# Optimization experiments

Measured on AMD Instinct MI355X. Metric: run time of the kernel, lower is better.

The kernel has to match this reference:

```python
import jax, jax.numpy as jnp
import numpy as np

B, T_MEM, T_TGT = 32, 256, 128
E = H = 512          # embed_size == hidden_size == memory feature dim (required by module math)
V = 10000            # vocab size


def setup_inputs() -> dict:
    key = jax.random.key(0)
    ks = jax.random.split(key, 10)
    s = 0.05
    return {
        "memory": jax.random.normal(ks[0], (B, T_MEM, E), dtype=jnp.float32),
        "tgt": jax.random.randint(ks[1], (B, T_TGT), 0, V),
        "emb_in": jax.random.normal(ks[2], (V, E), dtype=jnp.float32) * s,
        "W_ih": jax.random.normal(ks[3], (4 * H, E + H), dtype=jnp.float32) * s,
        "W_hh": jax.random.normal(ks[4], (4 * H, H), dtype=jnp.float32) * s,
        "b_ih": jax.random.normal(ks[5], (4 * H,), dtype=jnp.float32) * s,
        "b_hh": jax.random.normal(ks[6], (4 * H,), dtype=jnp.float32) * s,
        "W_out": jax.random.normal(ks[7], (V, H), dtype=jnp.float32) * s,
        "b_out": jax.random.normal(ks[8], (V,), dtype=jnp.float32) * s,
    }


def reference(memory, tgt, emb_in, W_ih, W_hh, b_ih, b_hh, W_out, b_out):
    # memory: (B, T_mem, E); tgt: (B, T_tgt) int
    Bq, Tm, Ed = memory.shape
    Hd = W_hh.shape[1]
    scale = 1.0 / jnp.sqrt(jnp.asarray(Ed, dtype=memory.dtype))

    x_emb = emb_in[tgt]                       # (B, T_tgt, E) teacher-forced inputs
    x_seq = jnp.swapaxes(x_emb, 0, 1)         # (T_tgt, B, E) for scan

    def step(carry, x_t):
        h, c = carry                          # (B, H), (B, H)
        # scaled dot-product attention: query=h, keys=values=memory
        scores = jnp.einsum('be,bte->bt', h, memory) * scale
        attn = jax.nn.softmax(scores, axis=-1)
        context = jnp.einsum('bt,bte->be', attn, memory)   # (B, E)
        inp = jnp.concatenate([context, x_t], axis=-1)     # (B, E + E_embed)
        gates = inp @ W_ih.T + b_ih + h @ W_hh.T + b_hh    # (B, 4H)
        i, f, g, o = jnp.split(gates, 4, axis=-1)          # torch LSTMCell gate order
        c_new = jax.nn.sigmoid(f) * c + jax.nn.sigmoid(i) * jnp.tanh(g)
        h_new = jax.nn.sigmoid(o) * jnp.tanh(c_new)
        logits = h_new @ W_out.T + b_out                   # (B, V)
        return (h_new, c_new), logits

    h0 = jnp.zeros((Bq, Hd), dtype=memory.dtype)
    c0 = jnp.zeros((Bq, Hd), dtype=memory.dtype)
    _, logits_seq = jax.lax.scan(step, (h0, c0), x_seq)    # (T_tgt, B, V)
    return jnp.swapaxes(logits_seq, 0, 1)                  # (B, T_tgt, V)
```

## Files before the change

### kernel.cpp

```cpp
#include <hip/hip_runtime.h>
#include <stdint.h>

#define TT 128

typedef __attribute__((ext_vector_type(8))) short short8;
typedef __attribute__((ext_vector_type(4))) float f32x4;
typedef __attribute__((ext_vector_type(4))) uint32_t u32x4;

__device__ __forceinline__ float blo(uint32_t u){ union{uint32_t i; float f;} v; v.i = u << 16; return v.f; }
__device__ __forceinline__ float bhi(uint32_t u){ union{uint32_t i; float f;} v; v.i = u & 0xffff0000u; return v.f; }
__device__ __forceinline__ float bf2f(uint16_t u){ union{uint32_t i; float f;} v; v.i = ((uint32_t)u) << 16; return v.f; }
__device__ __forceinline__ uint16_t f2bf(float f){
  union{float f; uint32_t i;} v; v.f = f;
  uint32_t r = v.i + 0x7fffu + ((v.i >> 16) & 1u);
  return (uint16_t)(r >> 16);
}
__device__ __forceinline__ uint32_t bfpack(float a, float b) {
  return (uint32_t)f2bf(a) | ((uint32_t)f2bf(b) << 16);
}
__device__ __forceinline__ void xstore(uint32_t* p, uint32_t v) {
  __hip_atomic_store(p, v, __ATOMIC_RELAXED, __HIP_MEMORY_SCOPE_AGENT);
}
__device__ __forceinline__ uint32_t xload(const uint32_t* p) {
  return __hip_atomic_load(p, __ATOMIC_RELAXED, __HIP_MEMORY_SCOPE_AGENT);
}
__device__ __forceinline__ void xstore64(unsigned long long* p, unsigned long long v) {
  __hip_atomic_store(p, v, __ATOMIC_RELAXED, __HIP_MEMORY_SCOPE_AGENT);
}
__device__ __forceinline__ unsigned long long xload64(const unsigned long long* p) {
  return __hip_atomic_load(p, __ATOMIC_RELAXED, __HIP_MEMORY_SCOPE_AGENT);
}
__device__ __forceinline__ void xstoref(float* p, float v) {
  __hip_atomic_store(p, v, __ATOMIC_RELAXED, __HIP_MEMORY_SCOPE_AGENT);
}
__device__ __forceinline__ float xloadf(const float* p) {
  return __hip_atomic_load(p, __ATOMIC_RELAXED, __HIP_MEMORY_SCOPE_AGENT);
}

__global__ __launch_bounds__(256) void k_prep_mem(const float* __restrict__ mem,
                                                  uint32_t* __restrict__ memK,
                                                  uint32_t* __restrict__ memT) {
  int idx = blockIdx.x * 256 + threadIdx.x;
  if (idx < 2097152) {
    int e2 = idx & 255, k = (idx >> 8) & 255, b = idx >> 16;
    const float* p = mem + ((size_t)(b * 256 + k)) * 512 + e2 * 2;
    memK[idx] = bfpack(p[0], p[1]);
  } else {
    int j = idx - 2097152;
    int k = j & 255, e2 = (j >> 8) & 255, b = j >> 16;
    const float* p = mem + ((size_t)(b * 256 + k)) * 512 + e2 * 2;
    memT[j] = bfpack(p[0], p[1]);
  }
}

__global__ __launch_bounds__(256) void k_prep_wsl(const float* __restrict__ W_ih, const float* __restrict__ W_hh,
                                                  uint32_t* __restrict__ Wsl) {
  int idx = blockIdx.x * 256 + threadIdx.x;
  int kk = idx & 3, t = (idx >> 2) & 255, kc = (idx >> 10) & 127, s = idx >> 17;
  int j = (t & 3) * 512 + s * 64 + (t >> 2);
  int k0 = kc * 8 + kk * 2;
  float w0 = (k0 < 512) ? W_ih[(size_t)j * 1024 + k0] : W_hh[(size_t)j * 512 + (k0 - 512)];
  float w1 = (k0 + 1 < 512) ? W_ih[(size_t)j * 1024 + k0 + 1] : W_hh[(size_t)j * 512 + (k0 + 1 - 512)];
  Wsl[idx] = bfpack(w0, w1);
}

__global__ __launch_bounds__(256) void k_prep_wx(const float* __restrict__ W_ih,
                                                 const float* __restrict__ b_ih, const float* __restrict__ b_hh,
                                                 uint16_t* __restrict__ Wxp, float* __restrict__ biasp) {
  int idx = blockIdx.x * 256 + threadIdx.x;
  int k = idx & 511, j = idx >> 9;
  Wxp[idx] = f2bf(W_ih[(size_t)j * 1024 + 512 + k]);
  if (k == 0) biasp[j] = b_ih[j] + b_hh[j];
}

__global__ __launch_bounds__(256) void k_prep_wo(const float* __restrict__ W_out, uint16_t* __restrict__ WoP) {
  int idx = blockIdx.x * 256 + threadIdx.x;
  if (idx < 5120000) WoP[idx] = f2bf(W_out[idx]);
  else WoP[idx] = 0;
}

__global__ __launch_bounds__(256) void k_gather_x(const float* __restrict__ emb, const int* __restrict__ tgt,
                                                  uint16_t* __restrict__ Axg) {
  int idx = blockIdx.x * 256 + threadIdx.x;
  int k = idx & 511, m = idx >> 9;
  Axg[idx] = f2bf(emb[(size_t)tgt[m] * 512 + k]);
}

template<int MODE>
__global__ __launch_bounds__(256) void gemm_bt(const uint16_t* __restrict__ A, const uint16_t* __restrict__ B,
                                               const float* __restrict__ bias, void* __restrict__ Cout,
                                               int K, int Nreal, int ldc, int tilesN) {
  __shared__ __align__(16) uint16_t As[128 * 32];
  __shared__ __align__(16) uint16_t Bs[128 * 32];
  const int tid = threadIdx.x;
  const int wv = tid >> 6, lane = tid & 63;
  const int tm = blockIdx.x / tilesN, tn = blockIdx.x % tilesN;
  const int wr = wv >> 1, wc = wv & 1;

  f32x4 acc[4][4];
#pragma unroll
  for (int m = 0; m < 4; ++m)
#pragma unroll
    for (int n = 0; n < 4; ++n) acc[m][n] = (f32x4){0.f, 0.f, 0.f, 0.f};

  const int frow = lane & 15;
  const int fk = (lane >> 4) << 3;
  const int srow = lane >> 2;
  const int skof = (lane & 3) << 3;

  const uint16_t* Abase = A + (size_t)tm * 128 * K;
  const uint16_t* Bbase = B + (size_t)tn * 128 * K;

  for (int k0 = 0; k0 < K; k0 += 32) {
    __syncthreads();
#pragma unroll
    for (int i = 0; i < 2; ++i) {
      const int chunk = wv * 2 + i;
      const int row = chunk * 16 + srow;
      const uint16_t* ga = Abase + (size_t)row * K + k0 + skof;
      const uint16_t* gb = Bbase + (size_t)row * K + k0 + skof;
      __builtin_amdgcn_global_load_lds((const __attribute__((address_space(1))) uint32_t*)(const void*)ga,
                                       (__attribute__((address_space(3))) uint32_t*)(void*)(As + chunk * 512),
                                       16, 0, 0);
      __builtin_amdgcn_global_load_lds((const __attribute__((address_space(1))) uint32_t*)(const void*)gb,
                                       (__attribute__((address_space(3))) uint32_t*)(void*)(Bs + chunk * 512),
                                       16, 0, 0);
    }
    __syncthreads();
    short8 af[4], bfr[4];
#pragma unroll
    for (int m = 0; m < 4; ++m) af[m] = *(const short8*)(As + (wr * 64 + m * 16 + frow) * 32 + fk);
#pragma unroll
    for (int n = 0; n < 4; ++n) bfr[n] = *(const short8*)(Bs + (wc * 64 + n * 16 + frow) * 32 + fk);
#pragma unroll
    for (int m = 0; m < 4; ++m)
#pragma unroll
      for (int n = 0; n < 4; ++n)
        acc[m][n] = __builtin_amdgcn_mfma_f32_16x16x32_bf16(af[m], bfr[n], acc[m][n], 0, 0, 0);
  }

  const int crow = (lane >> 4) << 2;
  const int ccol = lane & 15;
#pragma unroll
  for (int n = 0; n < 4; ++n) {
    const int gcol = tn * 128 + wc * 64 + n * 16 + ccol;
    if (gcol < Nreal) {
      const float bv = bias[gcol];
#pragma unroll
      for (int m = 0; m < 4; ++m) {
#pragma unroll
        for (int j = 0; j < 4; ++j) {
          const int grow = tm * 128 + wr * 64 + m * 16 + crow + j;
          const float v = acc[m][n][j] + bv;
          if (MODE == 0) ((float*)Cout)[(size_t)grow * ldc + gcol] = v;
          else {
            int q = gcol >> 9, r = gcol & 511;
            int pos = ((r >> 6) << 8) + ((r & 63) << 2) + q;
            ((uint16_t*)Cout)[(size_t)grow * ldc + pos] = f2bf(v);
          }
        }
      }
    }
  }
}

__global__ __launch_bounds__(512, 1) void recur_kernel(
    const uint32_t* __restrict__ memK, const uint32_t* __restrict__ memT,
    const uint32_t* __restrict__ Wsl, const uint16_t* __restrict__ Xgp,
    unsigned long long* __restrict__ ugl, float* __restrict__ zgl,
    uint32_t* __restrict__ hgl, uint16_t* __restrict__ hA, uint32_t* __restrict__ flags) {
  __shared__ __align__(16) uint32_t mTl[2][8192];
  __shared__ __align__(16) uint32_t mKl[2][8192];
  __shared__ __align__(16) uint32_t hx[2][256];
  __shared__ __align__(16) float xf[2][1024];
  __shared__ float red[256];
  __shared__ float rux[512], ruy[512];
  __shared__ float accs[512];
  __shared__ float el[32];

  const int g = blockIdx.x;
  const int s = g & 7, pp = g >> 3;
  const int tid = threadIdx.x;
  const int lane = tid & 63;
  const int wv = tid >> 6;
  const int sub = tid & 31, p = tid >> 5;
  const int row = tid & 255, half = tid >> 8;

  const uint32_t* wrow = Wsl + ((size_t)s << 17) + row * 4;

#pragma unroll
  for (int bi = 0; bi < 2; ++bi) {
    const int b = pp + bi * 16;
    const uint32_t* mTb = memT + ((size_t)b << 16);
    const uint32_t* mKb = memK + ((size_t)b << 16) + ((size_t)(32 * s) << 8);
    for (int j = tid; j < 8192; j += 512) {
      mKl[bi][j] = mKb[j];
      int e2 = j >> 5, kk = j & 31;
      mTl[bi][j] = mTb[e2 * 256 + 32 * s + kk];
    }
  }
  float c[2] = {0.f, 0.f};
  if (tid < 256) { hx[0][tid] = 0u; hx[1][tid] = 0u; }
  xf[0][tid] = 0.f; xf[0][512 + tid] = 0.f;
  xf[1][tid] = 0.f; xf[1][512 + tid] = 0.f;
  __syncthreads();

  for (int t = 0; t < TT; ++t) {
#pragma unroll
    for (int bi = 0; bi < 2; ++bi) {
      const int b = pp + bi * 16;
      {
        float sc = 0.f;
#pragma unroll
        for (int i = 0; i < 16; ++i) {
          uint32_t mw = mTl[bi][(p + (i << 4)) * 32 + sub];
          uint32_t hw = hx[bi][p + (i << 4)];
          sc = fmaf(blo(mw), blo(hw), sc);
          sc = fmaf(bhi(mw), bhi(hw), sc);
        }
        sc += __shfl_xor(sc, 32);
        if (lane < 32) red[wv * 32 + lane] = sc;
      }
      __syncthreads();
      if (tid < 32) {
        float sf = red[tid] + red[32 + tid] + red[64 + tid] + red[96 + tid]
                 + red[128 + tid] + red[160 + tid] + red[192 + tid] + red[224 + tid];
        float e = __expf(sf * 0.044194173824159216f);
        el[tid] = e;
        float z = e;
        z += __shfl_xor(z, 16); z += __shfl_xor(z, 8);
        z += __shfl_xor(z, 4);  z += __shfl_xor(z, 2); z += __shfl_xor(z, 1);
        if (tid == 0) xstoref(&zgl[(b << 3) + s], z);
      }
      __syncthreads();
      {
        float ux = 0.f, uy = 0.f;
        const int k0 = half * 16;
#pragma unroll
        for (int kk = 0; kk < 16; ++kk) {
          uint32_t mw = mKl[bi][(k0 + kk) * 256 + row];
          float e = el[k0 + kk];
          ux = fmaf(blo(mw), e, ux);
          uy = fmaf(bhi(mw), e, uy);
        }
        rux[tid] = ux; ruy[tid] = uy;
      }
      __syncthreads();
      if (tid < 256) {
        union { float f[2]; unsigned long long u; } pk;
        pk.f[0] = rux[tid] + rux[tid + 256];
        pk.f[1] = ruy[tid] + ruy[tid + 256];
        xstore64(&ugl[(((size_t)b << 3) + s << 8) + tid], pk.u);
      }
      __syncthreads();
      if (tid == 0) xstore(&flags[b * 32 + s], (uint32_t)(2 * t + 1));
    }
#pragma unroll
    for (int bi = 0; bi < 2; ++bi) {
      const int b = pp + bi * 16;
      if (tid < 64) {
        int v;
        do {
          __builtin_amdgcn_s_sleep(2);
          v = (tid < 8) ? (int)xload(&flags[b * 32 + tid]) : (2 * t + 1);
        } while (__any(v < 2 * t + 1));
      }
      __syncthreads();
      {
        float zsum = 0.f;
        if (tid < 256) {
#pragma unroll
          for (int q = 0; q < 8; ++q) zsum += xloadf(&zgl[(b << 3) + q]);
        }
        float ux = 0.f, uy = 0.f;
        const int q0 = half * 4;
#pragma unroll
        for (int q = 0; q < 4; ++q) {
          union { float f[2]; unsigned long long u; } pk;
          pk.u = xload64(&ugl[(((size_t)b << 3) + (q0 + q) << 8) + row]);
          ux += pk.f[0]; uy += pk.f[1];
        }
        rux[tid] = ux; ruy[tid] = uy;
        __syncthreads();
        if (tid < 256) {
          float rz = 1.f / zsum;
          xf[bi][2 * tid]     = (rux[tid] + rux[tid + 256]) * rz;
          xf[bi][2 * tid + 1] = (ruy[tid] + ruy[tid + 256]) * rz;
        }
      }
      __syncthreads();
      {
        float acc = (half == 0) ? bf2f(Xgp[((size_t)b * TT + t) * 2048 + (s << 8) + row]) : 0.f;
        const int kcb = half * 64;
#pragma unroll 8
        for (int j = 0; j < 64; ++j) {
          const int kc = kcb + j;
          u32x4 w4 = *(const u32x4*)(wrow + kc * 1024);
          f32x4 xa = *(const f32x4*)(xf[bi] + kc * 8);
          f32x4 xb = *(const f32x4*)(xf[bi] + kc * 8 + 4);
          acc = fmaf(blo(w4.x), xa.x, acc); acc = fmaf(bhi(w4.x), xa.y, acc);
          acc = fmaf(blo(w4.y), xa.z, acc); acc = fmaf(bhi(w4.y), xa.w, acc);
          acc = fmaf(blo(w4.z), xb.x, acc); acc = fmaf(bhi(w4.z), xb.y, acc);
          acc = fmaf(blo(w4.w), xb.z, acc); acc = fmaf(bhi(w4.w), xb.w, acc);
        }
        accs[tid] = acc;
      }
      __syncthreads();
      if (tid < 256) {
        float tot = accs[tid] + accs[tid + 256];
        int lbase = lane & ~3;
        float gi = __shfl(tot, lbase, 64);
        float gf = __shfl(tot, lbase + 1, 64);
        float gg = __shfl(tot, lbase + 2, 64);
        float go = __shfl(tot, lbase + 3, 64);
        c[bi] = (1.f / (1.f + __expf(-gf))) * c[bi] + (1.f / (1.f + __expf(-gi))) * tanhf(gg);
        float hn = (1.f / (1.f + __expf(-go))) * tanhf(c[bi]);
        float hn4 = __shfl(hn, (lane & ~7) + 4, 64);
        if ((tid & 7) == 0) {
          uint32_t hp = bfpack(hn, hn4);
          int r2 = (s << 5) + (tid >> 3);
          xstore(&hgl[(b << 8) + r2], hp);
          ((uint32_t*)hA)[((size_t)b * TT + t) * 256 + r2] = hp;
        }
      }
      __syncthreads();
      if (tid == 0) xstore(&flags[b * 32 + s], (uint32_t)(2 * t + 2));
    }
#pragma unroll
    for (int bi = 0; bi < 2; ++bi) {
      const int b = pp + bi * 16;
      if (tid < 64) {
        int v;
        do {
          __builtin_amdgcn_s_sleep(2);
          v = (tid < 8) ? (int)xload(&flags[b * 32 + tid]) : (2 * t + 2);
        } while (__any(v < 2 * t + 2));
      }
      __syncthreads();
      if (tid < 256) {
        uint32_t hp = xload(&hgl[(b << 8) + tid]);
        hx[bi][tid] = hp;
        xf[bi][512 + 2 * tid] = blo(hp);
        xf[bi][513 + 2 * tid] = bhi(hp);
      }
    }
    __syncthreads();
  }
}

extern "C" void kernel_launch(void* const* d_in, const int* in_sizes, int n_in,
                              void* d_out, int out_size, void* d_ws, size_t ws_size,
                              hipStream_t stream) {
  const float* memory = (const float*)d_in[0];
  const int*   tgt    = (const int*)d_in[1];
  const float* emb_in = (const float*)d_in[2];
  const float* W_ih   = (const float*)d_in[3];
  const float* W_hh   = (const float*)d_in[4];
  const float* b_ih   = (const float*)d_in[5];
  const float* b_hh   = (const float*)d_in[6];
  const float* W_out  = (const float*)d_in[7];
  const float* b_out  = (const float*)d_in[8];
  float* out = (float*)d_out;
  char* ws = (char*)d_ws;

  uint32_t* memK  = (uint32_t*)(ws);
  uint32_t* memT  = (uint32_t*)(ws + 8388608);
  uint32_t* Wsl   = (uint32_t*)(ws + 16777216);
  uint16_t* Wxp   = (uint16_t*)(ws + 20971520);
  float*    biasp = (float*)(ws + 23068672);
  uint16_t* WoP   = (uint16_t*)(ws + 23076864);
  uint16_t* Axg   = (uint16_t*)(ws + 33431552);
  uint16_t* Xgp   = (uint16_t*)(ws + 37625856);
  uint16_t* hA    = (uint16_t*)(ws + 54403072);
  uint32_t* hgl   = (uint32_t*)(ws + 58597376);
  float*    zgl   = (float*)(ws + 58630144);
  uint32_t* flags = (uint32_t*)(ws + 58662912);
  unsigned long long* ugl = (unsigned long long*)Axg;

  hipMemsetAsync(flags, 0, 4096, stream);

  k_prep_mem<<<16384, 256, 0, stream>>>(memory, memK, memT);
  k_prep_wsl<<<4096, 256, 0, stream>>>(W_ih, W_hh, Wsl);
  k_prep_wx<<<4096, 256, 0, stream>>>(W_ih, b_ih, b_hh, Wxp, biasp);
  k_prep_wo<<<20224, 256, 0, stream>>>(W_out, WoP);
  k_gather_x<<<8192, 256, 0, stream>>>(emb_in, tgt, Axg);

  gemm_bt<1><<<32 * 16, 256, 0, stream>>>(Axg, Wxp, biasp, Xgp, 512, 2048, 2048, 16);

  recur_kernel<<<128, 512, 0, stream>>>(memK, memT, Wsl, Xgp, ugl, zgl, hgl, hA, flags);

  gemm_bt<0><<<32 * 79, 256, 0, stream>>>(hA, WoP, b_out, out, 512, 10000, 10000, 79);
}
```

Measured before the change: 2.127 ms.

## Split recurrence across 256 blocks with shared LSTM weight pass for two batches

The persistent recurrence kernel now runs on 256 blocks instead of 128, each owning 16 memory rows and 32 hidden units for two batch rows. Memory is read straight from global/L2 rather than staged in LDS. The gate matvec is fused so each weight load serves both batch rows, halving weight traffic per block. The cost is twice as many blocks taking part in the cross-block flag synchronisation each step, plus uncached memory reads.

```diff
diff --git a/kernel.cpp b/kernel.cpp
--- a/kernel.cpp
+++ b/kernel.cpp
@@ -53,15 +53,15 @@
   }
 }
 
-__global__ __launch_bounds__(256) void k_prep_wsl(const float* __restrict__ W_ih, const float* __restrict__ W_hh,
-                                                  uint32_t* __restrict__ Wsl) {
+__global__ __launch_bounds__(256) void k_prep_wsl2(const float* __restrict__ W_ih, const float* __restrict__ W_hh,
+                                                   uint32_t* __restrict__ Wsl2) {
   int idx = blockIdx.x * 256 + threadIdx.x;
-  int kk = idx & 3, t = (idx >> 2) & 255, kc = (idx >> 10) & 127, s = idx >> 17;
-  int j = (t & 3) * 512 + s * 64 + (t >> 2);
+  int kk = idx & 3, t2 = (idx >> 2) & 127, kc = (idx >> 9) & 127, sg = idx >> 16;
+  int j = (t2 & 3) * 512 + sg * 32 + (t2 >> 2);
   int k0 = kc * 8 + kk * 2;
   float w0 = (k0 < 512) ? W_ih[(size_t)j * 1024 + k0] : W_hh[(size_t)j * 512 + (k0 - 512)];
   float w1 = (k0 + 1 < 512) ? W_ih[(size_t)j * 1024 + k0 + 1] : W_hh[(size_t)j * 512 + (k0 + 1 - 512)];
-  Wsl[idx] = bfpack(w0, w1);
+  Wsl2[idx] = bfpack(w0, w1);
 }
 
 __global__ __launch_bounds__(256) void k_prep_wx(const float* __restrict__ W_ih,
@@ -166,79 +166,75 @@
 
 __global__ __launch_bounds__(512, 1) void recur_kernel(
     const uint32_t* __restrict__ memK, const uint32_t* __restrict__ memT,
-    const uint32_t* __restrict__ Wsl, const uint16_t* __restrict__ Xgp,
+    const uint32_t* __restrict__ Wsl2, const uint16_t* __restrict__ Xgp,
     unsigned long long* __restrict__ ugl, float* __restrict__ zgl,
     uint32_t* __restrict__ hgl, uint16_t* __restrict__ hA, uint32_t* __restrict__ flags) {
-  __shared__ __align__(16) uint32_t mTl[2][8192];
-  __shared__ __align__(16) uint32_t mKl[2][8192];
   __shared__ __align__(16) uint32_t hx[2][256];
   __shared__ __align__(16) float xf[2][1024];
-  __shared__ float red[256];
+  __shared__ float red[128];
   __shared__ float rux[512], ruy[512];
-  __shared__ float accs[512];
-  __shared__ float el[32];
+  __shared__ float accsA[512], accsB[512];
+  __shared__ float el[16];
 
   const int g = blockIdx.x;
-  const int s = g & 7, pp = g >> 3;
+  const int sg = g & 15, pp = g >> 4;
+  const int b0 = pp, b1 = pp + 16;
   const int tid = threadIdx.x;
   const int lane = tid & 63;
   const int wv = tid >> 6;
-  const int sub = tid & 31, p = tid >> 5;
+  const int kl = tid & 15, eg = tid >> 4;
   const int row = tid & 255, half = tid >> 8;
-
-  const uint32_t* wrow = Wsl + ((size_t)s << 17) + row * 4;
-
-#pragma unroll
-  for (int bi = 0; bi < 2; ++bi) {
-    const int b = pp + bi * 16;
-    const uint32_t* mTb = memT + ((size_t)b << 16);
-    const uint32_t* mKb = memK + ((size_t)b << 16) + ((size_t)(32 * s) << 8);
-    for (int j = tid; j < 8192; j += 512) {
-      mKl[bi][j] = mKb[j];
-      int e2 = j >> 5, kk = j & 31;
-      mTl[bi][j] = mTb[e2 * 256 + 32 * s + kk];
-    }
-  }
-  float c[2] = {0.f, 0.f};
+  const int t2 = tid & 127, h4 = tid >> 7;
+
+  const uint32_t* wr2 = Wsl2 + ((size_t)sg << 16) + t2 * 4;
+  const int rD = 32 * sg + (t2 >> 2), qD = t2 & 3;
+  const int posD = ((rD >> 6) << 8) + ((rD & 63) << 2) + qD;
+
+  float cS = 0.f;
   if (tid < 256) { hx[0][tid] = 0u; hx[1][tid] = 0u; }
   xf[0][tid] = 0.f; xf[0][512 + tid] = 0.f;
   xf[1][tid] = 0.f; xf[1][512 + tid] = 0.f;
   __syncthreads();
 
   for (int t = 0; t < TT; ++t) {
+    const int T1 = 2 * t + 1, T2 = 2 * t + 2;
 #pragma unroll
     for (int bi = 0; bi < 2; ++bi) {
-      const int b = pp + bi * 16;
+      const int b = bi ? b1 : b0;
       {
+        const uint32_t* mA = memT + ((size_t)b << 16) + 16 * sg + kl;
         float sc = 0.f;
 #pragma unroll
-        for (int i = 0; i < 16; ++i) {
-          uint32_t mw = mTl[bi][(p + (i << 4)) * 32 + sub];
-          uint32_t hw = hx[bi][p + (i << 4)];
+        for (int i = 0; i < 8; ++i) {
+          uint32_t mw = mA[(size_t)(eg + (i << 5)) << 8];
+          uint32_t hw = hx[bi][eg + (i << 5)];
           sc = fmaf(blo(mw), blo(hw), sc);
           sc = fmaf(bhi(mw), bhi(hw), sc);
         }
+        sc += __shfl_xor(sc, 16);
         sc += __shfl_xor(sc, 32);
-        if (lane < 32) red[wv * 32 + lane] = sc;
-      }
-      __syncthreads();
-      if (tid < 32) {
-        float sf = red[tid] + red[32 + tid] + red[64 + tid] + red[96 + tid]
-                 + red[128 + tid] + red[160 + tid] + red[192 + tid] + red[224 + tid];
+        if (lane < 16) red[wv * 16 + lane] = sc;
+      }
+      __syncthreads();
+      if (tid < 16) {
+        float sf = 0.f;
+#pragma unroll
+        for (int w = 0; w < 8; ++w) sf += red[w * 16 + tid];
         float e = __expf(sf * 0.044194173824159216f);
         el[tid] = e;
         float z = e;
-        z += __shfl_xor(z, 16); z += __shfl_xor(z, 8);
-        z += __shfl_xor(z, 4);  z += __shfl_xor(z, 2); z += __shfl_xor(z, 1);
-        if (tid == 0) xstoref(&zgl[(b << 3) + s], z);
+        z += __shfl_xor(z, 8); z += __shfl_xor(z, 4);
+        z += __shfl_xor(z, 2); z += __shfl_xor(z, 1);
+        if (tid == 0) xstoref(&zgl[b * 16 + sg], z);
       }
       __syncthreads();
       {
+        const uint32_t* mC = memK + ((size_t)b << 16) + ((size_t)(16 * sg) << 8) + row;
         float ux = 0.f, uy = 0.f;
-        const int k0 = half * 16;
-#pragma unroll
-        for (int kk = 0; kk < 16; ++kk) {
-          uint32_t mw = mKl[bi][(k0 + kk) * 256 + row];
+        const int k0 = half * 8;
+#pragma unroll
+        for (int kk = 0; kk < 8; ++kk) {
+          uint32_t mw = mC[(size_t)(k0 + kk) << 8];
           float e = el[k0 + kk];
           ux = fmaf(blo(mw), e, ux);
           uy = fmaf(bhi(mw), e, uy);
@@ -250,34 +246,34 @@
         union { float f[2]; unsigned long long u; } pk;
         pk.f[0] = rux[tid] + rux[tid + 256];
         pk.f[1] = ruy[tid] + ruy[tid + 256];
-        xstore64(&ugl[(((size_t)b << 3) + s << 8) + tid], pk.u);
-      }
-      __syncthreads();
-      if (tid == 0) xstore(&flags[b * 32 + s], (uint32_t)(2 * t + 1));
+        xstore64(&ugl[(((size_t)b * 16 + sg) << 8) + tid], pk.u);
+      }
+      __syncthreads();
+      if (tid == 0) xstore(&flags[b * 32 + sg], (uint32_t)T1);
     }
 #pragma unroll
     for (int bi = 0; bi < 2; ++bi) {
-      const int b = pp + bi * 16;
+      const int b = bi ? b1 : b0;
       if (tid < 64) {
         int v;
         do {
           __builtin_amdgcn_s_sleep(2);
-          v = (tid < 8) ? (int)xload(&flags[b * 32 + tid]) : (2 * t + 1);
-        } while (__any(v < 2 * t + 1));
+          v = (tid < 16) ? (int)xload(&flags[b * 32 + tid]) : T1;
+        } while (__any(v < T1));
       }
       __syncthreads();
       {
         float zsum = 0.f;
         if (tid < 256) {
 #pragma unroll
-          for (int q = 0; q < 8; ++q) zsum += xloadf(&zgl[(b << 3) + q]);
+          for (int q = 0; q < 16; ++q) zsum += xloadf(&zgl[b * 16 + q]);
         }
         float ux = 0.f, uy = 0.f;
-        const int q0 = half * 4;
-#pragma unroll
-        for (int q = 0; q < 4; ++q) {
+        const int q0 = half * 8;
+#pragma unroll
+        for (int q = 0; q < 8; ++q) {
           union { float f[2]; unsigned long long u; } pk;
-          pk.u = xload64(&ugl[(((size_t)b << 3) + (q0 + q) << 8) + row]);
+          pk.u = xload64(&ugl[(((size_t)b * 16 + q0 + q) << 8) + row]);
           ux += pk.f[0]; uy += pk.f[1];
         }
         rux[tid] = ux; ruy[tid] = uy;
@@ -289,52 +285,65 @@
         }
       }
       __syncthreads();
-      {
-        float acc = (half == 0) ? bf2f(Xgp[((size_t)b * TT + t) * 2048 + (s << 8) + row]) : 0.f;
-        const int kcb = half * 64;
+    }
+    {
+      float accA = (h4 == 0) ? bf2f(Xgp[((size_t)(b0 * TT + t)) * 2048 + posD]) : 0.f;
+      float accB = (h4 == 0) ? bf2f(Xgp[((size_t)(b1 * TT + t)) * 2048 + posD]) : 0.f;
+      const int kc0 = h4 * 32;
 #pragma unroll 8
-        for (int j = 0; j < 64; ++j) {
-          const int kc = kcb + j;
-          u32x4 w4 = *(const u32x4*)(wrow + kc * 1024);
-          f32x4 xa = *(const f32x4*)(xf[bi] + kc * 8);
-          f32x4 xb = *(const f32x4*)(xf[bi] + kc * 8 + 4);
-          acc = fmaf(blo(w4.x), xa.x, acc); acc = fmaf(bhi(w4.x), xa.y, acc);
-          acc = fmaf(blo(w4.y), xa.z, acc); acc = fmaf(bhi(w4.y), xa.w, acc);
-          acc = fmaf(blo(w4.z), xb.x, acc); acc = fmaf(bhi(w4.z), xb.y, acc);
-          acc = fmaf(blo(w4.w), xb.z, acc); acc = fmaf(bhi(w4.w), xb.w, acc);
-        }
-        accs[tid] = acc;
-      }
-      __syncthreads();
-      if (tid < 256) {
-        float tot = accs[tid] + accs[tid + 256];
-        int lbase = lane & ~3;
-        float gi = __shfl(tot, lbase, 64);
-        float gf = __shfl(tot, lbase + 1, 64);
-        float gg = __shfl(tot, lbase + 2, 64);
-        float go = __shfl(tot, lbase + 3, 64);
-        c[bi] = (1.f / (1.f + __expf(-gf))) * c[bi] + (1.f / (1.f + __expf(-gi))) * tanhf(gg);
-        float hn = (1.f / (1.f + __expf(-go))) * tanhf(c[bi]);
-        float hn4 = __shfl(hn, (lane & ~7) + 4, 64);
-        if ((tid & 7) == 0) {
-          uint32_t hp = bfpack(hn, hn4);
-          int r2 = (s << 5) + (tid >> 3);
-          xstore(&hgl[(b << 8) + r2], hp);
-          ((uint32_t*)hA)[((size_t)b * TT + t) * 256 + r2] = hp;
-        }
-      }
-      __syncthreads();
-      if (tid == 0) xstore(&flags[b * 32 + s], (uint32_t)(2 * t + 2));
+      for (int j = 0; j < 32; ++j) {
+        const int kc = kc0 + j;
+        u32x4 w4 = *(const u32x4*)(wr2 + (size_t)kc * 512);
+        f32x4 xa = *(const f32x4*)(xf[0] + kc * 8);
+        f32x4 xb = *(const f32x4*)(xf[0] + kc * 8 + 4);
+        accA = fmaf(blo(w4.x), xa.x, accA); accA = fmaf(bhi(w4.x), xa.y, accA);
+        accA = fmaf(blo(w4.y), xa.z, accA); accA = fmaf(bhi(w4.y), xa.w, accA);
+        accA = fmaf(blo(w4.z), xb.x, accA); accA = fmaf(bhi(w4.z), xb.y, accA);
+        accA = fmaf(blo(w4.w), xb.z, accA); accA = fmaf(bhi(w4.w), xb.w, accA);
+        f32x4 ya = *(const f32x4*)(xf[1] + kc * 8);
+        f32x4 yb = *(const f32x4*)(xf[1] + kc * 8 + 4);
+        accB = fmaf(blo(w4.x), ya.x, accB); accB = fmaf(bhi(w4.x), ya.y, accB);
+        accB = fmaf(blo(w4.y), ya.z, accB); accB = fmaf(bhi(w4.y), ya.w, accB);
+        accB = fmaf(blo(w4.z), yb.x, accB); accB = fmaf(bhi(w4.z), yb.y, accB);
+        accB = fmaf(blo(w4.w), yb.z, accB); accB = fmaf(bhi(w4.w), yb.w, accB);
+      }
+      accsA[tid] = accA; accsB[tid] = accB;
+    }
+    __syncthreads();
+    if (tid < 256) {
+      const int bi = tid >> 7, t2e = tid & 127;
+      const int b = bi ? b1 : b0;
+      float tot = bi ? (accsB[t2e] + accsB[t2e + 128] + accsB[t2e + 256] + accsB[t2e + 384])
+                     : (accsA[t2e] + accsA[t2e + 128] + accsA[t2e + 256] + accsA[t2e + 384]);
+      int lbase = lane & ~3;
+      float gi = __shfl(tot, lbase, 64);
+      float gf = __shfl(tot, lbase + 1, 64);
+      float gg = __shfl(tot, lbase + 2, 64);
+      float go = __shfl(tot, lbase + 3, 64);
+      cS = (1.f / (1.f + __expf(-gf))) * cS + (1.f / (1.f + __expf(-gi))) * tanhf(gg);
+      float hn = (1.f / (1.f + __expf(-go))) * tanhf(cS);
+      float hn4 = __shfl(hn, (lane & ~7) + 4, 64);
+      if ((tid & 7) == 0) {
+        uint32_t hp = bfpack(hn, hn4);
+        int r2 = 16 * sg + (t2e >> 3);
+        xstore(&hgl[(b << 8) + r2], hp);
+        ((uint32_t*)hA)[((size_t)b * TT + t) * 256 + r2] = hp;
+      }
+    }
+    __syncthreads();
+    if (tid == 0) {
+      xstore(&flags[b0 * 32 + sg], (uint32_t)T2);
+      xstore(&flags[b1 * 32 + sg], (uint32_t)T2);
     }
 #pragma unroll
     for (int bi = 0; bi < 2; ++bi) {
-      const int b = pp + bi * 16;
+      const int b = bi ? b1 : b0;
       if (tid < 64) {
         int v;
         do {
           __builtin_amdgcn_s_sleep(2);
-          v = (tid < 8) ? (int)xload(&flags[b * 32 + tid]) : (2 * t + 2);
-        } while (__any(v < 2 * t + 2));
+          v = (tid < 16) ? (int)xload(&flags[b * 32 + tid]) : T2;
+        } while (__any(v < T2));
       }
       __syncthreads();
       if (tid < 256) {
@@ -343,8 +352,8 @@
         xf[bi][512 + 2 * tid] = blo(hp);
         xf[bi][513 + 2 * tid] = bhi(hp);
       }
-    }
-    __syncthreads();
+      __syncthreads();
+    }
   }
 }
 
@@ -365,7 +374,7 @@
 
   uint32_t* memK  = (uint32_t*)(ws);
   uint32_t* memT  = (uint32_t*)(ws + 8388608);
-  uint32_t* Wsl   = (uint32_t*)(ws + 16777216);
+  uint32_t* Wsl2  = (uint32_t*)(ws + 16777216);
   uint16_t* Wxp   = (uint16_t*)(ws + 20971520);
   float*    biasp = (float*)(ws + 23068672);
   uint16_t* WoP   = (uint16_t*)(ws + 23076864);
@@ -380,14 +389,14 @@
   hipMemsetAsync(flags, 0, 4096, stream);
 
   k_prep_mem<<<16384, 256, 0, stream>>>(memory, memK, memT);
-  k_prep_wsl<<<4096, 256, 0, stream>>>(W_ih, W_hh, Wsl);
+  k_prep_wsl2<<<4096, 256, 0, stream>>>(W_ih, W_hh, Wsl2);
   k_prep_wx<<<4096, 256, 0, stream>>>(W_ih, b_ih, b_hh, Wxp, biasp);
   k_prep_wo<<<20224, 256, 0, stream>>>(W_out, WoP);
   k_gather_x<<<8192, 256, 0, stream>>>(emb_in, tgt, Axg);
 
   gemm_bt<1><<<32 * 16, 256, 0, stream>>>(Axg, Wxp, biasp, Xgp, 512, 2048, 2048, 16);
 
-  recur_kernel<<<128, 512, 0, stream>>>(memK, memT, Wsl, Xgp, ugl, zgl, hgl, hA, flags);
+  recur_kernel<<<256, 512, 0, stream>>>(memK, memT, Wsl2, Xgp, ugl, zgl, hgl, hA, flags);
 
   gemm_bt<0><<<32 * 79, 256, 0, stream>>>(hA, WoP, b_out, out, 512, 10000, 10000, 79);
 }
```

After: 1.865 ms (median of 2 runs). 12.3% less time.
